# Kernel optimization log

Hardware: AMD Instinct MI355X
Metric: run time of the kernel (lower is better)

## Reference

```python
import jax, jax.numpy as jnp
import numpy as np

B, GH, GW, DIM, NH = 1, 48, 64, 1536, 16
HD = DIM // NH          # 96
C = HD // 2             # 48, divisible by 3 as the rope split requires
L = max(GH, GW)


def setup_inputs() -> dict:
    key = jax.random.key(0)
    ks = jax.random.split(key, 6)
    x = jax.random.normal(ks[0], (B, GH * GW, DIM), jnp.float32)
    w_init = lambda k: jax.random.normal(k, (DIM, DIM), jnp.float32) * 0.02
    # rope frequency table: theta[p, j] = p / 10000^(j/C); freqs = exp(i*theta)
    pos = jnp.arange(L, dtype=jnp.float32)[:, None]
    inv = 10000.0 ** (-jnp.arange(C, dtype=jnp.float32) / C)
    theta = pos * inv[None, :]
    return {
        "x": x,
        "wq": w_init(ks[1]), "bq": jnp.zeros((DIM,), jnp.float32),
        "wk": w_init(ks[2]), "bk": jnp.zeros((DIM,), jnp.float32),
        "wv": w_init(ks[3]), "bv": jnp.zeros((DIM,), jnp.float32),
        "wo": w_init(ks[4]), "bo": jnp.zeros((DIM,), jnp.float32),
        "freqs_cos": jnp.cos(theta), "freqs_sin": jnp.sin(theta),
        "h": GH, "w": GW,
    }


def rope_apply_spatial(x, freqs_cos, freqs_sin, h, w):
    # x: [b, s, n, d] with s == h*w. Complex rotation done in real arithmetic.
    b, s, n, d = x.shape
    c = d // 2
    c3 = c // 3
    # channel groups: [0:c3] identity (ones), [c3:2c3] rotated by h-position,
    # [2c3:3c3] rotated by w-position  (matches freqs.split + cat in torch)
    cos_hw = jnp.concatenate([
        jnp.ones((h, w, c3), x.dtype),
        jnp.broadcast_to(freqs_cos[:h, None, c3:2 * c3], (h, w, c3)),
        jnp.broadcast_to(freqs_cos[None, :w, 2 * c3:3 * c3], (h, w, c3)),
    ], axis=-1).reshape(1, s, 1, c)
    sin_hw = jnp.concatenate([
        jnp.zeros((h, w, c3), x.dtype),
        jnp.broadcast_to(freqs_sin[:h, None, c3:2 * c3], (h, w, c3)),
        jnp.broadcast_to(freqs_sin[None, :w, 2 * c3:3 * c3], (h, w, c3)),
    ], axis=-1).reshape(1, s, 1, c)
    xc = x.reshape(b, s, n, c, 2)
    xr, xi = xc[..., 0], xc[..., 1]
    yr = xr * cos_hw - xi * sin_hw
    yi = xr * sin_hw + xi * cos_hw
    return jnp.stack([yr, yi], axis=-1).reshape(b, s, n, d)


def reference(x, wq, bq, wk, bk, wv, bv, wo, bo, freqs_cos, freqs_sin, h, w):
    b, s, _ = x.shape
    q = (x @ wq + bq).reshape(b, s, NH, HD)
    k = (x @ wk + bk).reshape(b, s, NH, HD)
    v = (x @ wv + bv).reshape(b, s, NH, HD)
    q = rope_apply_spatial(q, freqs_cos, freqs_sin, h, w)
    k = rope_apply_spatial(k, freqs_cos, freqs_sin, h, w)
    scale = 1.0 / jnp.sqrt(jnp.asarray(HD, q.dtype))
    scores = jnp.einsum('bqnd,bknd->bnqk', q, k) * scale  # [b, n, s, s]
    attn = jax.nn.softmax(scores, axis=-1)
    out = jnp.einsum('bnqk,bknd->bqnd', attn, v).reshape(b, s, NH * HD)
    return out @ wo + bo
```

## Files before the change

### kernel.cpp

```cpp
#include <hip/hip_runtime.h>
#include <math.h>

#define S_LEN 3072
#define DIM 1536
#define NHEADS 16
#define HDIM 96
#define NPAIR 48

typedef __attribute__((ext_vector_type(8))) _Float16 half8;
typedef __attribute__((ext_vector_type(4))) _Float16 half4v;
typedef __attribute__((ext_vector_type(2))) _Float16 half2v;
typedef __attribute__((ext_vector_type(4))) float f32x4;

__device__ inline void gload16(const void* g, void* l) {
    __builtin_amdgcn_global_load_lds(
        (const __attribute__((address_space(1))) void*)g,
        (__attribute__((address_space(3))) void*)l, 16, 0, 0);
}

__device__ inline unsigned int packh2(float a, float b) {
    _Float16 ha = (_Float16)a, hb = (_Float16)b;
    unsigned short ua = *(unsigned short*)&ha;
    unsigned short ub = *(unsigned short*)&hb;
    return (unsigned int)ua | ((unsigned int)ub << 16);
}

__global__ __launch_bounds__(256)
void convert_f32_f16(const float* __restrict__ src, _Float16* __restrict__ dst, int n4)
{
    int i = blockIdx.x * 256 + threadIdx.x;
    if (i < n4) {
        float4 v = *(const float4*)&src[(size_t)i * 4];
        half4v h = { (_Float16)v.x, (_Float16)v.y, (_Float16)v.z, (_Float16)v.w };
        *(half4v*)&dst[(size_t)i * 4] = h;
    }
}

__global__ __launch_bounds__(256)
void transpose_w(const float* __restrict__ w0, const float* __restrict__ w1,
                 const float* __restrict__ w2, const float* __restrict__ w3,
                 _Float16* __restrict__ wt)
{
    __shared__ _Float16 t[64][68];
    const int z = blockIdx.z;
    const float* W = (z == 0) ? w0 : (z == 1) ? w1 : (z == 2) ? w2 : w3;
    _Float16* O = wt + (size_t)z * DIM * DIM;
    const int k0 = blockIdx.y * 64, n0 = blockIdx.x * 64;
    const int tid = threadIdx.x;
    const int r = tid >> 4, c4 = (tid & 15) * 4;
#pragma unroll
    for (int g = 0; g < 4; g++) {
        int kk = r + g * 16;
        float4 v = *(const float4*)&W[(size_t)(k0 + kk) * DIM + n0 + c4];
        t[c4 + 0][kk] = (_Float16)v.x; t[c4 + 1][kk] = (_Float16)v.y;
        t[c4 + 2][kk] = (_Float16)v.z; t[c4 + 3][kk] = (_Float16)v.w;
    }
    __syncthreads();
    const int nr = tid >> 2, ks = (tid & 3) * 16;
#pragma unroll
    for (int s = 0; s < 4; s++)
        *(ushort4*)&O[(size_t)(n0 + nr) * DIM + k0 + ks + s * 4] =
            *(ushort4*)&t[nr][ks + s * 4];
}

template<bool QKV>
__global__ __launch_bounds__(256)
void gemm_f16(const _Float16* __restrict__ X,
              const _Float16* __restrict__ W0t, const _Float16* __restrict__ W1t,
              const _Float16* __restrict__ W2t,
              const float* __restrict__ B0, const float* __restrict__ B1,
              const float* __restrict__ B2,
              const float* __restrict__ fc, const float* __restrict__ fs,
              void* __restrict__ outv)
{
    __shared__ __align__(16) _Float16 As[128][64];
    __shared__ __align__(16) _Float16 Bs[128][64];

    const int tid = threadIdx.x;
    const int w = tid >> 6, lane = tid & 63;
    const int ln = lane & 15, quad = lane >> 4;
    const int bz = blockIdx.z;
    const _Float16* Wt = W0t; const float* bias = B0;
    if (QKV) { if (bz == 1) { Wt = W1t; bias = B1; } else if (bz == 2) { Wt = W2t; bias = B2; } }
    const int m0 = blockIdx.y * 128, n0 = blockIdx.x * 128;
    const int wm = w >> 1, wn = w & 1;
    const int row8 = lane >> 3, cch = lane & 7;
    const int gch = cch ^ row8;

    f32x4 acc[4][4];
#pragma unroll
    for (int i = 0; i < 4; i++)
#pragma unroll
        for (int j = 0; j < 4; j++) acc[i][j] = (f32x4){0.f, 0.f, 0.f, 0.f};

    for (int k0 = 0; k0 < DIM; k0 += 64) {
        __syncthreads();
#pragma unroll
        for (int j = 0; j < 4; j++) {
            const int r = w * 32 + j * 8;
            gload16(X  + (size_t)(m0 + r + row8) * DIM + k0 + gch * 8, &As[r][0]);
            gload16(Wt + (size_t)(n0 + r + row8) * DIM + k0 + gch * 8, &Bs[r][0]);
        }
        __syncthreads();

        half8 a[4][2], b[4][2];
#pragma unroll
        for (int mt = 0; mt < 4; mt++) {
            int m = wm * 64 + mt * 16 + ln;
#pragma unroll
            for (int ks = 0; ks < 2; ks++) {
                int s = (ks * 4 + quad) ^ (ln & 7);
                a[mt][ks] = *(const half8*)&As[m][s * 8];
            }
        }
#pragma unroll
        for (int nt = 0; nt < 4; nt++) {
            int n = wn * 64 + nt * 16 + ln;
#pragma unroll
            for (int ks = 0; ks < 2; ks++) {
                int s = (ks * 4 + quad) ^ (ln & 7);
                b[nt][ks] = *(const half8*)&Bs[n][s * 8];
            }
        }
#pragma unroll
        for (int ks = 0; ks < 2; ks++)
#pragma unroll
            for (int mt = 0; mt < 4; mt++)
#pragma unroll
                for (int nt = 0; nt < 4; nt++)
                    acc[mt][nt] = __builtin_amdgcn_mfma_f32_16x16x32_f16(
                        a[mt][ks], b[nt][ks], acc[mt][nt], 0, 0, 0);
    }

#pragma unroll
    for (int nt = 0; nt < 4; nt++) {
        int col = n0 + wn * 64 + nt * 16 + ln;
        float bv = bias[col];
        int head = col / HDIM, hd = col % HDIM;
        int jc = hd >> 1;
        bool isreal = (ln & 1) == 0;
#pragma unroll
        for (int mt = 0; mt < 4; mt++) {
            int row0 = m0 + wm * 64 + mt * 16 + quad * 4;
            if (QKV && bz == 2) {
                half4v p;
#pragma unroll
                for (int r = 0; r < 4; r++) p[r] = (_Float16)(acc[mt][nt][r] + bv);
                *(half4v*)&((_Float16*)outv)[(((size_t)2 * NHEADS + head) * HDIM + hd) * S_LEN + row0] = p;
            } else if (QKV) {
                float v[4], vp[4];
#pragma unroll
                for (int r = 0; r < 4; r++) v[r] = acc[mt][nt][r] + bv;
#pragma unroll
                for (int r = 0; r < 4; r++) vp[r] = __shfl_xor(v[r], 1);
#pragma unroll
                for (int r = 0; r < 4; r++) {
                    int srow = row0 + r;
                    int pos = (jc < 32) ? (srow >> 6) : (srow & 63);
                    float c  = fc[pos * NPAIR + jc];
                    float sn = fs[pos * NPAIR + jc];
                    float xr = isreal ? v[r] : vp[r];
                    float xi = isreal ? vp[r] : v[r];
                    float rot = isreal ? (xr * c - xi * sn) : (xr * sn + xi * c);
                    float outval = (jc < 16) ? v[r] : rot;
                    ((_Float16*)outv)[(((size_t)bz * NHEADS + head) * S_LEN + srow) * HDIM + hd]
                        = (_Float16)outval;
                }
            } else {
#pragma unroll
                for (int r = 0; r < 4; r++)
                    ((float*)outv)[(size_t)(row0 + r) * DIM + col] = acc[mt][nt][r] + bv;
            }
        }
    }
}

__global__ __launch_bounds__(128, 2)
void attn_mfma_kernel(const _Float16* __restrict__ qh, const _Float16* __restrict__ kh,
                      const _Float16* __restrict__ vtg, _Float16* __restrict__ aoh)
{
    __shared__ __align__(16) _Float16 Ks[64][104];
    __shared__ __align__(16) _Float16 Vt[96][64];
    __shared__ __align__(16) _Float16 Pl[4][16][72];

    const int tid  = threadIdx.x;
    const int wid  = tid >> 6;
    const int lane = tid & 63;
    const int ln   = lane & 15;
    const int quad = lane >> 4;
    const int h    = blockIdx.y;
    const int q0   = blockIdx.x * 64;
    const float scale_ = 0.10206207261596577f;
    const int NT = S_LEN / 64;

    half8 aq[2][3];
#pragma unroll
    for (int qs = 0; qs < 2; qs++) {
        const _Float16* qrow = qh + (((size_t)h * S_LEN) + q0 + (wid * 2 + qs) * 16 + ln) * HDIM;
#pragma unroll
        for (int kb3 = 0; kb3 < 3; kb3++) {
            half8 a = *(const half8*)&qrow[kb3 * 32 + quad * 8];
            half8 v;
#pragma unroll
            for (int i = 0; i < 8; i++) v[i] = (_Float16)((float)a[i] * scale_);
            aq[qs][kb3] = v;
        }
    }

    f32x4 o[2][6];
#pragma unroll
    for (int qs = 0; qs < 2; qs++)
#pragma unroll
        for (int dn = 0; dn < 6; dn++) o[qs][dn] = (f32x4){0.f, 0.f, 0.f, 0.f};
    float m_[2] = {-INFINITY, -INFINITY}, l_[2] = {0.f, 0.f};

    const _Float16* kbase = kh + ((size_t)h * S_LEN) * HDIM;
    const _Float16* vbase = vtg + ((size_t)h * HDIM) * S_LEN;

    const int krow = tid >> 1, kc0 = (tid & 1) * 6;
    const _Float16* ksrc0 = kbase + (size_t)krow * HDIM + kc0 * 8;
    _Float16* kdst = &Ks[krow][kc0 * 8];
    const int vd0 = tid >> 3, vc = tid & 7;
    const _Float16* vsrc0 = vbase + (size_t)vd0 * S_LEN + vc * 8;
    _Float16* vdst = &Vt[vd0][(vc ^ (vd0 & 7)) * 8];

    uint4 kp0, kp1, kp2, kp3, kp4, kp5, vp0, vp1, vp2, vp3, vp4, vp5;
    kp0 = *(const uint4*)(ksrc0 + 0 * 8);  kp1 = *(const uint4*)(ksrc0 + 1 * 8);
    kp2 = *(const uint4*)(ksrc0 + 2 * 8);  kp3 = *(const uint4*)(ksrc0 + 3 * 8);
    kp4 = *(const uint4*)(ksrc0 + 4 * 8);  kp5 = *(const uint4*)(ksrc0 + 5 * 8);
    vp0 = *(const uint4*)(vsrc0 + 0 * 16 * S_LEN);
    vp1 = *(const uint4*)(vsrc0 + 1 * 16 * S_LEN);
    vp2 = *(const uint4*)(vsrc0 + 2 * 16 * S_LEN);
    vp3 = *(const uint4*)(vsrc0 + 3 * 16 * S_LEN);
    vp4 = *(const uint4*)(vsrc0 + 4 * 16 * S_LEN);
    vp5 = *(const uint4*)(vsrc0 + 5 * 16 * S_LEN);

    for (int kt = 0; kt < NT; ++kt) {
        __syncthreads();
        *(uint4*)(kdst + 0 * 8) = kp0;  *(uint4*)(kdst + 1 * 8) = kp1;
        *(uint4*)(kdst + 2 * 8) = kp2;  *(uint4*)(kdst + 3 * 8) = kp3;
        *(uint4*)(kdst + 4 * 8) = kp4;  *(uint4*)(kdst + 5 * 8) = kp5;
        *(uint4*)(vdst + 0 * 16 * 64) = vp0;  *(uint4*)(vdst + 1 * 16 * 64) = vp1;
        *(uint4*)(vdst + 2 * 16 * 64) = vp2;  *(uint4*)(vdst + 3 * 16 * 64) = vp3;
        *(uint4*)(vdst + 4 * 16 * 64) = vp4;  *(uint4*)(vdst + 5 * 16 * 64) = vp5;
        __syncthreads();

        if (kt + 1 < NT) {
            const _Float16* ks2 = ksrc0 + (size_t)(kt + 1) * 64 * HDIM;
            const _Float16* vs2 = vsrc0 + (kt + 1) * 64;
            kp0 = *(const uint4*)(ks2 + 0 * 8);  kp1 = *(const uint4*)(ks2 + 1 * 8);
            kp2 = *(const uint4*)(ks2 + 2 * 8);  kp3 = *(const uint4*)(ks2 + 3 * 8);
            kp4 = *(const uint4*)(ks2 + 4 * 8);  kp5 = *(const uint4*)(ks2 + 5 * 8);
            vp0 = *(const uint4*)(vs2 + 0 * 16 * S_LEN);
            vp1 = *(const uint4*)(vs2 + 1 * 16 * S_LEN);
            vp2 = *(const uint4*)(vs2 + 2 * 16 * S_LEN);
            vp3 = *(const uint4*)(vs2 + 3 * 16 * S_LEN);
            vp4 = *(const uint4*)(vs2 + 4 * 16 * S_LEN);
            vp5 = *(const uint4*)(vs2 + 5 * 16 * S_LEN);
        }

        f32x4 s[2][4];
#pragma unroll
        for (int nb = 0; nb < 4; nb++) {
            half8 ak0 = *(const half8*)&Ks[nb * 16 + ln][0 * 32 + quad * 8];
            half8 ak1 = *(const half8*)&Ks[nb * 16 + ln][1 * 32 + quad * 8];
            half8 ak2 = *(const half8*)&Ks[nb * 16 + ln][2 * 32 + quad * 8];
#pragma unroll
            for (int qs = 0; qs < 2; qs++) {
                f32x4 acc = (f32x4){0.f, 0.f, 0.f, 0.f};
                acc = __builtin_amdgcn_mfma_f32_16x16x32_f16(ak0, aq[qs][0], acc, 0, 0, 0);
                acc = __builtin_amdgcn_mfma_f32_16x16x32_f16(ak1, aq[qs][1], acc, 0, 0, 0);
                acc = __builtin_amdgcn_mfma_f32_16x16x32_f16(ak2, aq[qs][2], acc, 0, 0, 0);
                s[qs][nb] = acc;
            }
        }

        float al[2];
#pragma unroll
        for (int qs = 0; qs < 2; qs++) {
            float mx = s[qs][0][0];
#pragma unroll
            for (int nb = 0; nb < 4; nb++)
#pragma unroll
                for (int r = 0; r < 4; r++) mx = fmaxf(mx, s[qs][nb][r]);
            mx = fmaxf(mx, __shfl_xor(mx, 16));
            mx = fmaxf(mx, __shfl_xor(mx, 32));
            float mn = fmaxf(m_[qs], mx);
            al[qs] = __expf(m_[qs] - mn);
            m_[qs] = mn;
            float rs = 0.f;
#pragma unroll
            for (int nb = 0; nb < 4; nb++)
#pragma unroll
                for (int r = 0; r < 4; r++) {
                    float p = __expf(s[qs][nb][r] - mn);
                    s[qs][nb][r] = p;
                    rs += p;
                }
            rs += __shfl_xor(rs, 16);
            rs += __shfl_xor(rs, 32);
            l_[qs] = l_[qs] * al[qs] + rs;

#pragma unroll
            for (int nb = 0; nb < 4; nb++) {
                uint2 u;
                u.x = packh2(s[qs][nb][0], s[qs][nb][1]);
                u.y = packh2(s[qs][nb][2], s[qs][nb][3]);
                *(uint2*)&Pl[wid * 2 + qs][ln][nb * 16 + quad * 4] = u;
            }
#pragma unroll
            for (int dn = 0; dn < 6; dn++)
#pragma unroll
                for (int r = 0; r < 4; r++) o[qs][dn][r] *= al[qs];
        }

        half8 ap[2][2];
#pragma unroll
        for (int qs = 0; qs < 2; qs++)
#pragma unroll
            for (int c = 0; c < 2; c++)
                ap[qs][c] = *(const half8*)&Pl[wid * 2 + qs][ln][c * 32 + quad * 8];
#pragma unroll
        for (int c = 0; c < 2; c++) {
#pragma unroll
            for (int dn = 0; dn < 6; dn++) {
                int row = dn * 16 + ln;
                int slot = (c * 4 + quad) ^ (ln & 7);
                half8 av = *(const half8*)&Vt[row][slot * 8];
                o[0][dn] = __builtin_amdgcn_mfma_f32_16x16x32_f16(av, ap[0][c], o[0][dn], 0, 0, 0);
                o[1][dn] = __builtin_amdgcn_mfma_f32_16x16x32_f16(av, ap[1][c], o[1][dn], 0, 0, 0);
            }
        }
    }

#pragma unroll
    for (int qs = 0; qs < 2; qs++) {
        const float invl = 1.f / l_[qs];
        const size_t rowbase = (size_t)(q0 + (wid * 2 + qs) * 16 + ln) * DIM + h * HDIM;
#pragma unroll
        for (int dn = 0; dn < 6; dn++) {
            half4v p;
#pragma unroll
            for (int r = 0; r < 4; r++) p[r] = (_Float16)(o[qs][dn][r] * invl);
            *(half4v*)&aoh[rowbase + dn * 16 + quad * 4] = p;
        }
    }
}

extern "C" void kernel_launch(void* const* d_in, const int* in_sizes, int n_in,
                              void* d_out, int out_size, void* d_ws, size_t ws_size,
                              hipStream_t stream) {
    const float* x  = (const float*)d_in[0];
    const float* wq = (const float*)d_in[1];
    const float* bq = (const float*)d_in[2];
    const float* wk = (const float*)d_in[3];
    const float* bk = (const float*)d_in[4];
    const float* wv = (const float*)d_in[5];
    const float* bv = (const float*)d_in[6];
    const float* wo = (const float*)d_in[7];
    const float* bo = (const float*)d_in[8];
    const float* fc = (const float*)d_in[9];
    const float* fs = (const float*)d_in[10];
    float* out = (float*)d_out;

    const size_t per  = (size_t)NHEADS * S_LEN * HDIM;
    const size_t dim2 = (size_t)DIM * DIM;
    _Float16* hws  = (_Float16*)d_ws;
    _Float16* qkvh = hws;
    _Float16* qh   = qkvh;
    _Float16* kh   = qkvh + per;
    _Float16* vth  = qkvh + 2 * per;
    _Float16* xh   = hws + 3 * per;
    _Float16* wth  = hws + 4 * per;

    convert_f32_f16<<<(int)((S_LEN * DIM / 4 + 255) / 256), 256, 0, stream>>>(
        x, xh, S_LEN * DIM / 4);
    transpose_w<<<dim3(DIM / 64, DIM / 64, 4), 256, 0, stream>>>(wq, wk, wv, wo, wth);

    gemm_f16<true><<<dim3(DIM / 128, S_LEN / 128, 3), 256, 0, stream>>>(
        xh, wth, wth + dim2, wth + 2 * dim2, bq, bk, bv, fc, fs, qkvh);
    attn_mfma_kernel<<<dim3(S_LEN / 64, NHEADS), 128, 0, stream>>>(qh, kh, vth, xh);
    gemm_f16<false><<<dim3(DIM / 128, S_LEN / 128, 1), 256, 0, stream>>>(
        xh, wth + 3 * dim2, nullptr, nullptr, bo, nullptr, nullptr, fc, fs, out);
}
```

Measured before the change: 336.3 us.

## Split attention KV range across two blocks with combine kernel, swizzle LDS, use exp2

Adds a split-KV mode: each query tile's key range is divided in two blocks (grid z=2) that write unnormalized fp32 partial outputs plus max/sum, merged by a new combine kernel. This doubles the number of attention blocks (768 to 1536) for better CU occupancy, and launch bounds are raised to 3 waves per SIMD. It also removes LDS padding in favor of XOR/rotation swizzles for K and P tiles, and folds log2(e) into the Q scale so exp2 replaces expf. The cost is extra fp32 partial traffic, an extra launch, and a fallback path if the workspace is too small.

```diff
diff --git a/kernel.cpp b/kernel.cpp
--- a/kernel.cpp
+++ b/kernel.cpp
@@ -175,13 +175,15 @@
     }
 }
 
-__global__ __launch_bounds__(128, 2)
+template<bool SPLIT>
+__global__ __launch_bounds__(128, 3)
 void attn_mfma_kernel(const _Float16* __restrict__ qh, const _Float16* __restrict__ kh,
-                      const _Float16* __restrict__ vtg, _Float16* __restrict__ aoh)
+                      const _Float16* __restrict__ vtg, _Float16* __restrict__ aoh,
+                      float* __restrict__ Opart, float* __restrict__ Ml)
 {
-    __shared__ __align__(16) _Float16 Ks[64][104];
+    __shared__ __align__(16) _Float16 Ks[64][96];
     __shared__ __align__(16) _Float16 Vt[96][64];
-    __shared__ __align__(16) _Float16 Pl[4][16][72];
+    __shared__ __align__(16) _Float16 Pl[4][16][64];
 
     const int tid  = threadIdx.x;
     const int wid  = tid >> 6;
@@ -190,8 +192,9 @@
     const int quad = lane >> 4;
     const int h    = blockIdx.y;
     const int q0   = blockIdx.x * 64;
-    const float scale_ = 0.10206207261596577f;
-    const int NT = S_LEN / 64;
+    const int sp   = SPLIT ? blockIdx.z : 0;
+    const int NT   = SPLIT ? (S_LEN / 64 / 2) : (S_LEN / 64);
+    const float scale2 = 0.14724511850021248f;
 
     half8 aq[2][3];
 #pragma unroll
@@ -202,7 +205,7 @@
             half8 a = *(const half8*)&qrow[kb3 * 32 + quad * 8];
             half8 v;
 #pragma unroll
-            for (int i = 0; i < 8; i++) v[i] = (_Float16)((float)a[i] * scale_);
+            for (int i = 0; i < 8; i++) v[i] = (_Float16)((float)a[i] * scale2);
             aq[qs][kb3] = v;
         }
     }
@@ -214,15 +217,19 @@
         for (int dn = 0; dn < 6; dn++) o[qs][dn] = (f32x4){0.f, 0.f, 0.f, 0.f};
     float m_[2] = {-INFINITY, -INFINITY}, l_[2] = {0.f, 0.f};
 
-    const _Float16* kbase = kh + ((size_t)h * S_LEN) * HDIM;
-    const _Float16* vbase = vtg + ((size_t)h * HDIM) * S_LEN;
+    const _Float16* kbase = kh + ((size_t)h * S_LEN + sp * NT * 64) * HDIM;
+    const _Float16* vbase = vtg + ((size_t)h * HDIM) * S_LEN + sp * NT * 64;
 
     const int krow = tid >> 1, kc0 = (tid & 1) * 6;
+    const int fsw = (krow >> 1) & 3;
     const _Float16* ksrc0 = kbase + (size_t)krow * HDIM + kc0 * 8;
-    _Float16* kdst = &Ks[krow][kc0 * 8];
+    _Float16* krb = &Ks[krow][0];
     const int vd0 = tid >> 3, vc = tid & 7;
     const _Float16* vsrc0 = vbase + (size_t)vd0 * S_LEN + vc * 8;
     _Float16* vdst = &Vt[vd0][(vc ^ (vd0 & 7)) * 8];
+
+    const int qk = (quad + ((ln >> 1) & 3)) & 3;
+    const int psw = ln & 7;
 
     uint4 kp0, kp1, kp2, kp3, kp4, kp5, vp0, vp1, vp2, vp3, vp4, vp5;
     kp0 = *(const uint4*)(ksrc0 + 0 * 8);  kp1 = *(const uint4*)(ksrc0 + 1 * 8);
@@ -237,9 +244,15 @@
 
     for (int kt = 0; kt < NT; ++kt) {
         __syncthreads();
-        *(uint4*)(kdst + 0 * 8) = kp0;  *(uint4*)(kdst + 1 * 8) = kp1;
-        *(uint4*)(kdst + 2 * 8) = kp2;  *(uint4*)(kdst + 3 * 8) = kp3;
-        *(uint4*)(kdst + 4 * 8) = kp4;  *(uint4*)(kdst + 5 * 8) = kp5;
+        {
+            int c, p;
+            c = kc0 + 0; p = (c & ~3) | ((c + fsw) & 3); *(uint4*)&krb[p * 8] = kp0;
+            c = kc0 + 1; p = (c & ~3) | ((c + fsw) & 3); *(uint4*)&krb[p * 8] = kp1;
+            c = kc0 + 2; p = (c & ~3) | ((c + fsw) & 3); *(uint4*)&krb[p * 8] = kp2;
+            c = kc0 + 3; p = (c & ~3) | ((c + fsw) & 3); *(uint4*)&krb[p * 8] = kp3;
+            c = kc0 + 4; p = (c & ~3) | ((c + fsw) & 3); *(uint4*)&krb[p * 8] = kp4;
+            c = kc0 + 5; p = (c & ~3) | ((c + fsw) & 3); *(uint4*)&krb[p * 8] = kp5;
+        }
         *(uint4*)(vdst + 0 * 16 * 64) = vp0;  *(uint4*)(vdst + 1 * 16 * 64) = vp1;
         *(uint4*)(vdst + 2 * 16 * 64) = vp2;  *(uint4*)(vdst + 3 * 16 * 64) = vp3;
         *(uint4*)(vdst + 4 * 16 * 64) = vp4;  *(uint4*)(vdst + 5 * 16 * 64) = vp5;
@@ -262,9 +275,10 @@
         f32x4 s[2][4];
 #pragma unroll
         for (int nb = 0; nb < 4; nb++) {
-            half8 ak0 = *(const half8*)&Ks[nb * 16 + ln][0 * 32 + quad * 8];
-            half8 ak1 = *(const half8*)&Ks[nb * 16 + ln][1 * 32 + quad * 8];
-            half8 ak2 = *(const half8*)&Ks[nb * 16 + ln][2 * 32 + quad * 8];
+            const _Float16* kr = &Ks[nb * 16 + ln][0];
+            half8 ak0 = *(const half8*)&kr[(0 * 4 + qk) * 8];
+            half8 ak1 = *(const half8*)&kr[(1 * 4 + qk) * 8];
+            half8 ak2 = *(const half8*)&kr[(2 * 4 + qk) * 8];
 #pragma unroll
             for (int qs = 0; qs < 2; qs++) {
                 f32x4 acc = (f32x4){0.f, 0.f, 0.f, 0.f};
@@ -286,14 +300,14 @@
             mx = fmaxf(mx, __shfl_xor(mx, 16));
             mx = fmaxf(mx, __shfl_xor(mx, 32));
             float mn = fmaxf(m_[qs], mx);
-            al[qs] = __expf(m_[qs] - mn);
+            al[qs] = __builtin_amdgcn_exp2f(m_[qs] - mn);
             m_[qs] = mn;
             float rs = 0.f;
 #pragma unroll
             for (int nb = 0; nb < 4; nb++)
 #pragma unroll
                 for (int r = 0; r < 4; r++) {
-                    float p = __expf(s[qs][nb][r] - mn);
+                    float p = __builtin_amdgcn_exp2f(s[qs][nb][r] - mn);
                     s[qs][nb][r] = p;
                     rs += p;
                 }
@@ -306,7 +320,8 @@
                 uint2 u;
                 u.x = packh2(s[qs][nb][0], s[qs][nb][1]);
                 u.y = packh2(s[qs][nb][2], s[qs][nb][3]);
-                *(uint2*)&Pl[wid * 2 + qs][ln][nb * 16 + quad * 4] = u;
+                int ph = (2 * nb + (quad >> 1)) ^ psw;
+                *(uint2*)&Pl[wid * 2 + qs][ln][ph * 8 + (quad & 1) * 4] = u;
             }
 #pragma unroll
             for (int dn = 0; dn < 6; dn++)
@@ -318,8 +333,10 @@
 #pragma unroll
         for (int qs = 0; qs < 2; qs++)
 #pragma unroll
-            for (int c = 0; c < 2; c++)
-                ap[qs][c] = *(const half8*)&Pl[wid * 2 + qs][ln][c * 32 + quad * 8];
+            for (int c = 0; c < 2; c++) {
+                int ph = (4 * c + quad) ^ psw;
+                ap[qs][c] = *(const half8*)&Pl[wid * 2 + qs][ln][ph * 8];
+            }
 #pragma unroll
         for (int c = 0; c < 2; c++) {
 #pragma unroll
@@ -335,16 +352,56 @@
 
 #pragma unroll
     for (int qs = 0; qs < 2; qs++) {
-        const float invl = 1.f / l_[qs];
-        const size_t rowbase = (size_t)(q0 + (wid * 2 + qs) * 16 + ln) * DIM + h * HDIM;
-#pragma unroll
-        for (int dn = 0; dn < 6; dn++) {
-            half4v p;
-#pragma unroll
-            for (int r = 0; r < 4; r++) p[r] = (_Float16)(o[qs][dn][r] * invl);
-            *(half4v*)&aoh[rowbase + dn * 16 + quad * 4] = p;
-        }
-    }
+        const int row = q0 + (wid * 2 + qs) * 16 + ln;
+        if (SPLIT) {
+            const size_t obase = (((size_t)sp * NHEADS + h) * S_LEN + row) * HDIM;
+#pragma unroll
+            for (int dn = 0; dn < 6; dn++) {
+                float4 p = { o[qs][dn][0], o[qs][dn][1], o[qs][dn][2], o[qs][dn][3] };
+                *(float4*)&Opart[obase + dn * 16 + quad * 4] = p;
+            }
+            if (quad == 0) {
+                const size_t mlrow = (size_t)h * S_LEN + row;
+                Ml[((size_t)sp * 2 + 0) * NHEADS * S_LEN + mlrow] = m_[qs];
+                Ml[((size_t)sp * 2 + 1) * NHEADS * S_LEN + mlrow] = l_[qs];
+            }
+        } else {
+            const float invl = 1.f / l_[qs];
+            const size_t rowbase = (size_t)row * DIM + h * HDIM;
+#pragma unroll
+            for (int dn = 0; dn < 6; dn++) {
+                half4v p;
+#pragma unroll
+                for (int r = 0; r < 4; r++) p[r] = (_Float16)(o[qs][dn][r] * invl);
+                *(half4v*)&aoh[rowbase + dn * 16 + quad * 4] = p;
+            }
+        }
+    }
+}
+
+__global__ __launch_bounds__(256)
+void combine_kernel(const float* __restrict__ Opart, const float* __restrict__ Ml,
+                    _Float16* __restrict__ aoh)
+{
+    int idx = blockIdx.x * 256 + threadIdx.x;
+    int d4 = (idx % 24) * 4;
+    int row = idx / 24;
+    int h = row / S_LEN, q = row % S_LEN;
+    const size_t NS = (size_t)NHEADS * S_LEN;
+    float m1 = Ml[0 * NS + row], l1 = Ml[1 * NS + row];
+    float m2 = Ml[2 * NS + row], l2 = Ml[3 * NS + row];
+    float M = fmaxf(m1, m2);
+    float a1 = __builtin_amdgcn_exp2f(m1 - M);
+    float a2 = __builtin_amdgcn_exp2f(m2 - M);
+    float inv = 1.f / (a1 * l1 + a2 * l2);
+    float4 o1 = *(const float4*)&Opart[((size_t)row) * HDIM + d4];
+    float4 o2 = *(const float4*)&Opart[(NS + row) * HDIM + d4];
+    half4v p;
+    p[0] = (_Float16)((a1 * o1.x + a2 * o2.x) * inv);
+    p[1] = (_Float16)((a1 * o1.y + a2 * o2.y) * inv);
+    p[2] = (_Float16)((a1 * o1.z + a2 * o2.z) * inv);
+    p[3] = (_Float16)((a1 * o1.w + a2 * o2.w) * inv);
+    *(half4v*)&aoh[(size_t)q * DIM + h * HDIM + d4] = p;
 }
 
 extern "C" void kernel_launch(void* const* d_in, const int* in_sizes, int n_in,
@@ -366,20 +423,35 @@
     const size_t per  = (size_t)NHEADS * S_LEN * HDIM;
     const size_t dim2 = (size_t)DIM * DIM;
     _Float16* hws  = (_Float16*)d_ws;
-    _Float16* qkvh = hws;
-    _Float16* qh   = qkvh;
-    _Float16* kh   = qkvh + per;
-    _Float16* vth  = qkvh + 2 * per;
+    _Float16* qh   = hws;
+    _Float16* kh   = hws + per;
+    _Float16* vth  = hws + 2 * per;
     _Float16* xh   = hws + 3 * per;
     _Float16* wth  = hws + 4 * per;
+
+    const size_t baseHalves = 4 * per + 4 * dim2;
+    float* Opart = (float*)(hws + baseHalves);
+    float* Ml    = Opart + 2 * (size_t)NHEADS * S_LEN * HDIM;
+    const size_t needed = baseHalves * 2
+        + (2 * (size_t)NHEADS * S_LEN * HDIM + 4 * (size_t)NHEADS * S_LEN) * 4;
+    const bool use_split = ws_size >= needed;
 
     convert_f32_f16<<<(int)((S_LEN * DIM / 4 + 255) / 256), 256, 0, stream>>>(
         x, xh, S_LEN * DIM / 4);
     transpose_w<<<dim3(DIM / 64, DIM / 64, 4), 256, 0, stream>>>(wq, wk, wv, wo, wth);
 
     gemm_f16<true><<<dim3(DIM / 128, S_LEN / 128, 3), 256, 0, stream>>>(
-        xh, wth, wth + dim2, wth + 2 * dim2, bq, bk, bv, fc, fs, qkvh);
-    attn_mfma_kernel<<<dim3(S_LEN / 64, NHEADS), 128, 0, stream>>>(qh, kh, vth, xh);
+        xh, wth, wth + dim2, wth + 2 * dim2, bq, bk, bv, fc, fs, hws);
+
+    if (use_split) {
+        attn_mfma_kernel<true><<<dim3(S_LEN / 64, NHEADS, 2), 128, 0, stream>>>(
+            qh, kh, vth, nullptr, Opart, Ml);
+        combine_kernel<<<(NHEADS * S_LEN * 24) / 256, 256, 0, stream>>>(Opart, Ml, xh);
+    } else {
+        attn_mfma_kernel<false><<<dim3(S_LEN / 64, NHEADS, 1), 128, 0, stream>>>(
+            qh, kh, vth, xh, nullptr, nullptr);
+    }
+
     gemm_f16<false><<<dim3(DIM / 128, S_LEN / 128, 1), 256, 0, stream>>>(
         xh, wth + 3 * dim2, nullptr, nullptr, bo, nullptr, nullptr, fc, fs, out);
 }
```

New measurement: 362.2 us. 1.08x slower.
